# Kernel optimization log

Measured on AMD Instinct MI355X. Metric: run time of the kernel, lower is better.

The kernel has to match this reference:

```python
import jax, jax.numpy as jnp
import numpy as np

B, N, C_SA, OUT = 16, 2048, 512, 1024
BN_EPS = 1e-5


def pconv(x, w, b=None):
    # 1x1 Conv1d: x [B,Cin,N], w [Cout,Cin] -> [B,Cout,N]
    y = jnp.einsum('oc,bcn->bon', w, x)
    return y if b is None else y + b[None, :, None]


def setup_inputs() -> dict:
    key = jax.random.key(0)
    ks = jax.random.split(key, 16)
    s = lambda k, shape: jax.random.normal(k, shape, dtype=jnp.float32) * 0.05
    return {
        'x': jax.random.normal(ks[0], (B, 3, N), dtype=jnp.float32),
        'w1': s(ks[1], (128, 21)), 'b1': s(ks[2], (128,)),
        'w2': s(ks[3], (256, 128)), 'b2': s(ks[4], (256,)),
        'w3': s(ks[5], (512, 512)), 'b3': s(ks[6], (512,)),
        'w4': s(ks[7], (OUT, 512)), 'b4': s(ks[8], (OUT,)),
        'wqk': s(ks[9], (C_SA // 4, C_SA)),            # q_conv.weight tied to k_conv.weight, no bias
        'wv': s(ks[10], (C_SA, C_SA)), 'bv': s(ks[11], (C_SA,)),
        'wt': s(ks[12], (C_SA, C_SA)), 'bt': s(ks[13], (C_SA,)),
        'gamma': jnp.ones((C_SA,), dtype=jnp.float32),
        'beta': jnp.zeros((C_SA,), dtype=jnp.float32),
    }


def reference(x, w1, b1, w2, b2, w3, b3, w4, b4, wqk, wv, bv, wt, bt, gamma, beta):
    b, _, n = x.shape
    # positional encoding on [B,N,3]: [t, sin(t*2^i), cos(t*2^i)] for i in 0..2 -> 21 channels
    t = jnp.transpose(x, (0, 2, 1))
    enc = [t]
    for f in (1.0, 2.0, 4.0):
        enc.append(jnp.sin(t * f))
        enc.append(jnp.cos(t * f))
    h = jnp.transpose(jnp.concatenate(enc, axis=-1), (0, 2, 1))  # [B,21,N]

    h = jax.nn.relu(pconv(h, w1, b1))               # [B,128,N]
    h = pconv(h, w2, b2)                            # [B,256,N]
    g = jnp.max(h, axis=2)                          # [B,256]
    h = jnp.concatenate([h, jnp.broadcast_to(g[:, :, None], (b, g.shape[1], n))], axis=1)  # [B,512,N]
    h = jax.nn.relu(pconv(h, w3, b3))               # [B,512,N]

    # SA_Layer (offset attention, double normalization)
    xq = jnp.einsum('oc,bcn->bno', wqk, h)          # [B,N,128]
    xk = jnp.einsum('oc,bcn->bon', wqk, h)          # [B,128,N]
    xv = pconv(h, wv, bv)                           # [B,512,N]
    energy = jnp.einsum('bqo,bok->bqk', xq, xk)     # [B,N,N]
    attn = jax.nn.softmax(energy, axis=-1)
    attn = attn / (1e-9 + jnp.sum(attn, axis=1, keepdims=True))  # L1 renorm over query dim
    x_r = jnp.einsum('bck,bqk->bcq', xv, attn)      # x_v @ attn^T -> [B,512,N]
    d = pconv(h - x_r, wt, bt)
    # BatchNorm1d, training mode (batch statistics, biased variance)
    mu = jnp.mean(d, axis=(0, 2))
    var = jnp.var(d, axis=(0, 2))
    d = gamma[None, :, None] * (d - mu[None, :, None]) * jax.lax.rsqrt(var + BN_EPS)[None, :, None] + beta[None, :, None]
    h = h + jax.nn.relu(d)

    h = pconv(h, w4, b4)                            # [B,OUT,N]
    return jnp.max(h, axis=2)                       # [B,OUT]
```

## Files before the change

### kernel.cpp

```cpp
#include <hip/hip_runtime.h>
#include <cmath>

#define GN 2048
#define GB 16

typedef __attribute__((ext_vector_type(8))) short bf8_t;
typedef __attribute__((ext_vector_type(4))) float f4_t;

__device__ __forceinline__ short f2bf(float f) {
    union { float f; unsigned u; } v; v.f = f;
    unsigned r = v.u + 0x7FFFu + ((v.u >> 16) & 1u);
    return (short)(r >> 16);
}
__device__ __forceinline__ float bf2f(short s) {
    union { unsigned u; float f; } v; v.u = ((unsigned)(unsigned short)s) << 16;
    return v.f;
}

__device__ __forceinline__ void load16_lds(const short* g, short* l) {
    __builtin_amdgcn_global_load_lds(
        (const __attribute__((address_space(1))) unsigned int*)g,
        (__attribute__((address_space(3))) unsigned int*)l, 16, 0, 0);
}

__device__ __forceinline__ float wave_max(float v) {
#pragma unroll
    for (int o = 32; o > 0; o >>= 1) v = fmaxf(v, __shfl_xor(v, o, 64));
    return v;
}
__device__ __forceinline__ float wave_sum(float v) {
#pragma unroll
    for (int o = 32; o > 0; o >>= 1) v += __shfl_xor(v, o, 64);
    return v;
}
__device__ __forceinline__ float block_sum(float v) {
    __shared__ float sm[4];
    v = wave_sum(v);
    if ((threadIdx.x & 63) == 0) sm[threadIdx.x >> 6] = v;
    __syncthreads();
    v = sm[0] + sm[1] + sm[2] + sm[3];
    __syncthreads();
    return v;
}

__global__ __launch_bounds__(256) void f2ball_k(
    const float* __restrict__ w2, const float* __restrict__ w3,
    const float* __restrict__ wqk, const float* __restrict__ wv,
    const float* __restrict__ wt, const float* __restrict__ w4,
    short* __restrict__ dst) {
    int i = blockIdx.x * 256 + threadIdx.x;
    if (i >= 1409024) return;
    float v;
    if (i < 32768) v = w2[i];
    else if (i < 294912) v = w3[i - 32768];
    else if (i < 360448) v = wqk[i - 294912];
    else if (i < 622592) v = wv[i - 360448];
    else if (i < 884736) v = wt[i - 622592];
    else v = w4[i - 884736];
    dst[i] = f2bf(v);
}

__global__ __launch_bounds__(256) void posenc_conv1_k(
    const float* __restrict__ x, const float* __restrict__ w1,
    const float* __restrict__ b1, short* __restrict__ h1) {
    __shared__ float w[128 * 21];
    __shared__ float bb[128];
    __shared__ float se[256][21];
    const int tid = threadIdx.x;
    for (int i = tid; i < 128 * 21; i += 256) w[i] = w1[i];
    if (tid < 128) bb[tid] = b1[tid];
    int p0 = blockIdx.x * 256;
    int p = p0 + tid, b = p >> 11, n = p & (GN - 1);
    const float* xb = x + (long)b * 3 * GN + n;
    float t0 = xb[0], t1 = xb[GN], t2 = xb[2 * GN];
    se[tid][0] = t0; se[tid][1] = t1; se[tid][2] = t2;
    se[tid][3] = sinf(t0); se[tid][4] = sinf(t1); se[tid][5] = sinf(t2);
    se[tid][6] = cosf(t0); se[tid][7] = cosf(t1); se[tid][8] = cosf(t2);
    se[tid][9] = sinf(2.f * t0); se[tid][10] = sinf(2.f * t1); se[tid][11] = sinf(2.f * t2);
    se[tid][12] = cosf(2.f * t0); se[tid][13] = cosf(2.f * t1); se[tid][14] = cosf(2.f * t2);
    se[tid][15] = sinf(4.f * t0); se[tid][16] = sinf(4.f * t1); se[tid][17] = sinf(4.f * t2);
    se[tid][18] = cosf(4.f * t0); se[tid][19] = cosf(4.f * t1); se[tid][20] = cosf(4.f * t2);
    __syncthreads();
    short* outb = h1 + (long)p0 * 128;
    for (int it = 0; it < 128; ++it) {
        int L = it * 256 + tid;
        int pl = L >> 7, o = L & 127;
        float s = bb[o];
        const float* er = se[pl];
        const float* wr = &w[o * 21];
#pragma unroll
        for (int c = 0; c < 21; ++c) s = fmaf(wr[c], er[c], s);
        outb[L] = f2bf(fmaxf(s, 0.f));
    }
}

template <int MODE, int BIAS, bool RELU, bool STATS = false, bool COLMAX = false>
__global__ __launch_bounds__(256) void mm_k(
    const short* __restrict__ A, int lda, long long aB,
    const short* __restrict__ B, int ldb, long long bB,
    const float* __restrict__ bias, int biasStride,
    const short* __restrict__ aux, long long auxB,
    const float* __restrict__ rsv,
    float* __restrict__ Cf, long long cfB,
    short* __restrict__ Cb, long long cbB,
    float* __restrict__ Pmax, float* __restrict__ Ps2,
    int ldc, int K) {
    const int z = blockIdx.z;
    A += (long long)z * aB;
    B += (long long)z * bB;
    if (MODE == 4) { aux += (long long)z * auxB; rsv += (long long)z * GN; }
    if (MODE == 1) Cf += (long long)z * cfB;
    if (MODE == 2 || MODE == 4 || MODE == 6) Cb += (long long)z * cbB;
    if (MODE == 6) Pmax += (long long)z * GN * 32;
    const int row0 = blockIdx.x * 128, col0 = blockIdx.y * 128;
    const int tid = threadIdx.x;
    const int lane = tid & 63, w = tid >> 6;
    const int r = lane & 15, q = lane >> 4;
    const int wr = w >> 1, wc = w & 1;

    __shared__ short lA[8192];
    __shared__ short lB[8192];

    f4_t acc[4][4] = {};

    const int sRow = lane >> 2;
    const int sKb = (lane & 3) ^ ((lane >> 3) & 3);
    const long aG = (long)(row0 + w * 32 + sRow) * lda + sKb * 8;
    const long bG = (long)(col0 + w * 32 + sRow) * ldb + sKb * 8;
    short* ldsA0 = lA + (w * 32) * 32;
    short* ldsA1 = lA + (w * 32 + 16) * 32;
    short* ldsB0 = lB + (w * 32) * 32;
    short* ldsB1 = lB + (w * 32 + 16) * 32;

    const int sw = (q ^ ((r >> 1) & 3)) * 8;
    int aoff[4], boff[4];
#pragma unroll
    for (int i = 0; i < 4; ++i) {
        aoff[i] = (wr * 64 + i * 16 + r) * 32 + sw;
        boff[i] = (wc * 64 + i * 16 + r) * 32 + sw;
    }

    for (int k0 = 0; k0 < K; k0 += 64) {
        __syncthreads();
        load16_lds(A + aG + k0, ldsA0);
        load16_lds(A + aG + (long)16 * lda + k0, ldsA1);
        load16_lds(B + bG + k0, ldsB0);
        load16_lds(B + bG + (long)16 * ldb + k0, ldsB1);
        load16_lds(A + aG + k0 + 32, ldsA0 + 4096);
        load16_lds(A + aG + (long)16 * lda + k0 + 32, ldsA1 + 4096);
        load16_lds(B + bG + k0 + 32, ldsB0 + 4096);
        load16_lds(B + bG + (long)16 * ldb + k0 + 32, ldsB1 + 4096);
        asm volatile("s_waitcnt vmcnt(0)" ::: "memory");
        __syncthreads();
#pragma unroll
        for (int h = 0; h < 2; ++h) {
            const short* la = lA + h * 4096;
            const short* lb = lB + h * 4096;
            bf8_t av[4], bv[4];
#pragma unroll
            for (int i = 0; i < 4; ++i) av[i] = *(const bf8_t*)(la + aoff[i]);
#pragma unroll
            for (int j = 0; j < 4; ++j) bv[j] = *(const bf8_t*)(lb + boff[j]);
#pragma unroll
            for (int i = 0; i < 4; ++i)
#pragma unroll
                for (int j = 0; j < 4; ++j)
                    acc[i][j] = __builtin_amdgcn_mfma_f32_16x16x32_bf16(av[i], bv[j], acc[i][j], 0, 0, 0);
        }
    }

    if constexpr (MODE == 5) {
        int b = row0 >> 11;
        int rw = (blockIdx.x * 2 + wr) & 31;
#pragma unroll
        for (int j = 0; j < 4; ++j) {
            float vm = -1e30f;
#pragma unroll
            for (int i = 0; i < 4; ++i)
#pragma unroll
                for (int e = 0; e < 4; ++e) vm = fmaxf(vm, acc[i][j][e]);
            vm = fmaxf(vm, __shfl_xor(vm, 16, 64));
            vm = fmaxf(vm, __shfl_xor(vm, 32, 64));
            if (q == 0) {
                int gcol = col0 + wc * 64 + j * 16 + r;
                Pmax[(((long)b * 1024 + gcol) << 5) + rw] = vm + bias[gcol];
            }
        }
    } else if constexpr (MODE == 6) {
        float rsum[4][4] = {};
#pragma unroll
        for (int j = 0; j < 4; ++j) {
            int gcol = col0 + wc * 64 + j * 16 + r;
#pragma unroll
            for (int i = 0; i < 4; ++i) {
#pragma unroll
                for (int e = 0; e < 4; ++e) {
                    int grow = row0 + wr * 64 + i * 16 + q * 4 + e;
                    float ex = __expf(acc[i][j][e]);
                    rsum[i][e] += ex;
                    Cb[(long)grow * ldc + gcol] = f2bf(ex);
                }
            }
        }
#pragma unroll
        for (int i = 0; i < 4; ++i)
#pragma unroll
            for (int e = 0; e < 4; ++e) {
                float v = rsum[i][e];
                v += __shfl_xor(v, 1, 64);
                v += __shfl_xor(v, 2, 64);
                v += __shfl_xor(v, 4, 64);
                v += __shfl_xor(v, 8, 64);
                if (r == 0) {
                    int grow = row0 + wr * 64 + i * 16 + q * 4 + e;
                    Pmax[((long)grow << 5) + blockIdx.y * 2 + wc] = v;
                }
            }
    } else if constexpr (MODE == 4) {
#pragma unroll
        for (int i = 0; i < 4; ++i) {
#pragma unroll
            for (int e = 0; e < 4; ++e) {
                int grow = row0 + wr * 64 + i * 16 + q * 4 + e;
                float rsr = rsv[grow];
                long ob = (long)grow * ldc + col0 + wc * 64 + r;
#pragma unroll
                for (int j = 0; j < 4; ++j) {
                    long off = ob + j * 16;
                    Cb[off] = f2bf(bf2f(aux[off]) - acc[i][j][e] * rsr);
                }
            }
        }
    } else {
        const int b2d = (BIAS == 3) ? (row0 >> 11) : 0;
#pragma unroll
        for (int j = 0; j < 4; ++j) {
            int gcol = col0 + wc * 64 + j * 16 + r;
            float bvv = 0.f;
            if constexpr (BIAS == 1) bvv = bias[gcol];
            if constexpr (BIAS == 3) bvv = bias[b2d * biasStride + gcol];
            float s1 = 0.f, s2 = 0.f;
            float cmx = -1e30f;
#pragma unroll
            for (int i = 0; i < 4; ++i) {
#pragma unroll
                for (int e = 0; e < 4; ++e) {
                    int grow = row0 + wr * 64 + i * 16 + q * 4 + e;
                    float v = acc[i][j][e] + bvv;
                    if constexpr (BIAS == 2) v += bias[grow];
                    if constexpr (RELU) v = fmaxf(v, 0.f);
                    if constexpr (STATS) { s1 += v; s2 = fmaf(v, v, s2); }
                    if constexpr (COLMAX) cmx = fmaxf(cmx, v);
                    long off = (long)grow * ldc + gcol;
                    if constexpr (MODE == 1) Cf[off] = v;
                    if constexpr (MODE == 2) Cb[off] = f2bf(v);
                }
            }
            if constexpr (STATS) {
                s1 += __shfl_xor(s1, 16, 64); s1 += __shfl_xor(s1, 32, 64);
                s2 += __shfl_xor(s2, 16, 64); s2 += __shfl_xor(s2, 32, 64);
                if (q == 0) {
                    int rw2 = blockIdx.x * 2 + wr;
                    Pmax[rw2 * 512 + gcol] = s1;
                    Ps2[rw2 * 512 + gcol] = s2;
                }
            }
            if constexpr (COLMAX) {
                cmx = fmaxf(cmx, __shfl_xor(cmx, 16, 64));
                cmx = fmaxf(cmx, __shfl_xor(cmx, 32, 64));
                if (q == 0) {
                    int b = row0 >> 11;
                    int rw = (blockIdx.x * 2 + wr) & 31;
                    Pmax[(((long)b * ldc + gcol) << 5) + rw] = cmx;
                }
            }
        }
    }
}

__device__ __forceinline__ void stage2(const short* g0, const short* g1, short* dst) {
    load16_lds(g0, dst);
    load16_lds(g1, dst + 4096);
}

template <int MH, int NH>
__device__ __forceinline__ void mfma_quad(const bf8_t (&av)[4][2], const bf8_t (&bv)[2][2],
                                          f4_t (&acc)[8][4]) {
#pragma unroll
    for (int mi = 0; mi < 4; ++mi)
#pragma unroll
        for (int ni = 0; ni < 2; ++ni) {
            acc[MH * 4 + mi][NH * 2 + ni] = __builtin_amdgcn_mfma_f32_16x16x32_bf16(
                av[mi][0], bv[ni][0], acc[MH * 4 + mi][NH * 2 + ni], 0, 0, 0);
            acc[MH * 4 + mi][NH * 2 + ni] = __builtin_amdgcn_mfma_f32_16x16x32_bf16(
                av[mi][1], bv[ni][1], acc[MH * 4 + mi][NH * 2 + ni], 0, 0, 0);
        }
}

__device__ __forceinline__ void rd4(const short* p, int swz0, int swz1, bf8_t (&v)[4][2]) {
#pragma unroll
    for (int i = 0; i < 4; ++i) {
        v[i][0] = *(const bf8_t*)(p + i * 1024 + swz0);
        v[i][1] = *(const bf8_t*)(p + i * 1024 + swz1);
    }
}
__device__ __forceinline__ void rd2(const short* p, int swz0, int swz1, bf8_t (&v)[2][2]) {
#pragma unroll
    for (int i = 0; i < 2; ++i) {
        v[i][0] = *(const bf8_t*)(p + i * 1024 + swz0);
        v[i][1] = *(const bf8_t*)(p + i * 1024 + swz1);
    }
}

#define SB0 __builtin_amdgcn_sched_barrier(0)
#define BARRIER asm volatile("s_barrier" ::: "memory")

template <int MODE, int BIAS, bool RELU, bool STATS = false, bool SWZ = false>
__global__ __launch_bounds__(512, 2) void mm256_k(
    const short* __restrict__ A, int lda, long long aB,
    const short* __restrict__ B, int ldb, long long bB,
    const float* __restrict__ bias, int biasStride,
    const short* __restrict__ aux, long long auxB,
    const float* __restrict__ rsv,
    short* __restrict__ Cb, long long cbB,
    float* __restrict__ Pmax, float* __restrict__ Ps2,
    int ldc, int K) {
    __shared__ short lA[32768];
    __shared__ short lB[32768];
    int bx = blockIdx.x, by = blockIdx.y, bz = blockIdx.z;
    if constexpr (SWZ) {
        const int nwg = gridDim.x * gridDim.y * gridDim.z;
        const int bid = bx + gridDim.x * (by + gridDim.y * bz);
        const int cpx = nwg >> 3;
        const int wg = (bid & 7) * cpx + (bid >> 3);
        bx = wg % gridDim.x;
        const int t2 = wg / gridDim.x;
        by = t2 % gridDim.y;
        bz = t2 / gridDim.y;
    }
    const int z = bz;
    A += (long long)z * aB;
    B += (long long)z * bB;
    if constexpr (MODE == 4) { aux += (long long)z * auxB; rsv += (long long)z * GN; }
    if constexpr (MODE != 5) Cb += (long long)z * cbB;
    const int row0 = bx * 256, col0 = by * 256;
    const int tid = threadIdx.x;
    const int lane = tid & 63, w = tid >> 6;
    const int r16 = lane & 15, q = lane >> 4;
    const int wr = w >> 2, wc = w & 3;

    const int rc0 = w * 8 + (lane >> 3);
    const int s8 = ((lane & 7) ^ (rc0 & 7)) * 8;
    const long ldA64 = (long)64 * lda, ldB64 = (long)64 * ldb;
    const short* aH0 = A + (long)(row0 + rc0) * lda + s8;
    const short* aH1 = aH0 + (long)128 * lda;
    const short* bH0 = B + (long)(col0 + rc0) * ldb + s8;
    const short* bH1 = bH0 + (long)128 * ldb;
    short* dA = lA + w * 512;
    short* dB = lB + w * 512;

#define STG_A(d_, h_, kt_) stage2((h_ ? aH1 : aH0) + (long)(kt_) * 64,                      \
                                  (h_ ? aH1 : aH0) + (long)(kt_) * 64 + ldA64,              \
                                  dA + (d_) * 16384 + (h_) * 8192)
#define STG_B(d_, h_, kt_) stage2((h_ ? bH1 : bH0) + (long)(kt_) * 64,                      \
                                  (h_ ? bH1 : bH0) + (long)(kt_) * 64 + ldB64,              \
                                  dB + (d_) * 16384 + (h_) * 8192)

    const int swz0 = (q ^ (r16 & 7)) * 8;
    const int swz1 = ((4 + q) ^ (r16 & 7)) * 8;
    const int arow = (wr * 64 + r16) * 64;
    const int brow = (wc * 32 + r16) * 64;

    f4_t acc[8][4] = {};
    bf8_t av[4][2], bv0[2][2], bv1[2][2];
    const int NT = K >> 6;

    STG_A(0, 0, 0); STG_B(0, 0, 0); STG_B(0, 1, 0); STG_A(0, 1, 0);
    STG_A(1, 0, 1); STG_B(1, 0, 1);
    asm volatile("s_waitcnt vmcnt(4)" ::: "memory");
    SB0; BARRIER; SB0;

    for (int t = 0; t < NT; ++t) {
        const int d = t & 1;
        const short* la = lA + d * 16384;
        const short* lb = lB + d * 16384;
        rd4(la + arow, swz0, swz1, av);
        rd2(lb + brow, swz0, swz1, bv0);
        if (t + 1 < NT) STG_B(d ^ 1, 1, t + 1);
        SB0; BARRIER; SB0;
        __builtin_amdgcn_s_setprio(1);
        mfma_quad<0, 0>(av, bv0, acc);
        __builtin_amdgcn_s_setprio(0);
        SB0; BARRIER; SB0;
        rd2(lb + 8192 + brow, swz0, swz1, bv1);
        if (t + 1 < NT) STG_A(d ^ 1, 1, t + 1);
        SB0; BARRIER; SB0;
        __builtin_amdgcn_s_setprio(1);
        mfma_quad<0, 1>(av, bv1, acc);
        __builtin_amdgcn_s_setprio(0);
        SB0; BARRIER; SB0;
        rd4(la + 8192 + arow, swz0, swz1, av);
        if (t + 2 < NT) STG_A(d, 0, t + 2);
        SB0; BARRIER; SB0;
        __builtin_amdgcn_s_setprio(1);
        mfma_quad<1, 0>(av, bv0, acc);
        __builtin_amdgcn_s_setprio(0);
        SB0; BARRIER; SB0;
        if (t + 2 < NT) {
            STG_B(d, 0, t + 2);
            asm volatile("s_waitcnt vmcnt(4)" ::: "memory");
        } else if (t + 1 < NT) {
            asm volatile("s_waitcnt vmcnt(0)" ::: "memory");
        }
        SB0; BARRIER; SB0;
        __builtin_amdgcn_s_setprio(1);
        mfma_quad<1, 1>(av, bv1, acc);
        __builtin_amdgcn_s_setprio(0);
        SB0; BARRIER; SB0;
    }
#undef STG_A
#undef STG_B

    const int mrow = row0 + wr * 64 + q * 4;
    const int ncol = col0 + wc * 32 + r16;

    if constexpr (MODE == 4) {
#pragma unroll
        for (int m = 0; m < 8; ++m) {
#pragma unroll
            for (int e = 0; e < 4; ++e) {
                const int grow = mrow + (m >> 2) * 128 + (m & 3) * 16 + e;
                const float rsr = rsv[grow];
                const long rb = (long)grow * ldc;
#pragma unroll
                for (int n = 0; n < 4; ++n) {
                    const long off = rb + ncol + (n >> 1) * 128 + (n & 1) * 16;
                    Cb[off] = f2bf(bf2f(aux[off]) - acc[m][n][e] * rsr);
                }
            }
        }
    } else if constexpr (MODE == 2) {
        const int b2d = (BIAS == 3) ? (row0 >> 11) : 0;
#pragma unroll
        for (int n = 0; n < 4; ++n) {
            const int gcol = ncol + (n >> 1) * 128 + (n & 1) * 16;
            float bvv = 0.f;
            if constexpr (BIAS == 1) bvv = bias[gcol];
            if constexpr (BIAS == 3) bvv = bias[b2d * biasStride + gcol];
#pragma unroll
            for (int mh = 0; mh < 2; ++mh) {
                float s1 = 0.f, s2 = 0.f;
#pragma unroll
                for (int mi = 0; mi < 4; ++mi) {
#pragma unroll
                    for (int e = 0; e < 4; ++e) {
                        const int grow = mrow + mh * 128 + mi * 16 + e;
                        float v = acc[mh * 4 + mi][n][e] + bvv;
                        if constexpr (BIAS == 2) v += bias[grow];
                        if constexpr (RELU) v = fmaxf(v, 0.f);
                        if constexpr (STATS) { s1 += v; s2 = fmaf(v, v, s2); }
                        Cb[(long)grow * ldc + gcol] = f2bf(v);
                    }
                }
                if constexpr (STATS) {
                    s1 += __shfl_xor(s1, 16, 64); s1 += __shfl_xor(s1, 32, 64);
                    s2 += __shfl_xor(s2, 16, 64); s2 += __shfl_xor(s2, 32, 64);
                    if (q == 0) {
                        const int rw2 = bx * 4 + mh * 2 + wr;
                        Pmax[rw2 * 512 + gcol] = s1;
                        Ps2[rw2 * 512 + gcol] = s2;
                    }
                }
            }
        }
    } else if constexpr (MODE == 5) {
        const int b = row0 >> 11;
#pragma unroll
        for (int n = 0; n < 4; ++n) {
            const int gcol = ncol + (n >> 1) * 128 + (n & 1) * 16;
            const float bvv = bias[gcol];
#pragma unroll
            for (int mh = 0; mh < 2; ++mh) {
                float vm = -1e30f;
#pragma unroll
                for (int mi = 0; mi < 4; ++mi)
#pragma unroll
                    for (int e = 0; e < 4; ++e) vm = fmaxf(vm, acc[mh * 4 + mi][n][e]);
                vm = fmaxf(vm, __shfl_xor(vm, 16, 64));
                vm = fmaxf(vm, __shfl_xor(vm, 32, 64));
                if (q == 0) {
                    const int rw = (bx * 4 + mh * 2 + wr) & 31;
                    Pmax[(((long)b * ldc + gcol) << 5) + rw] = vm + bvv;
                }
            }
        }
    }
}
#undef SB0
#undef BARRIER

__global__ __launch_bounds__(256) void rs_k(const float* __restrict__ rp,
                                            float* __restrict__ rs) {
    int i = blockIdx.x * 256 + threadIdx.x;
    const float* p = rp + ((long)i << 5);
    float s = 0.f;
#pragma unroll
    for (int j = 0; j < 32; ++j) s += p[j];
    rs[i] = 1.f / s;
}

__global__ __launch_bounds__(256) void maxg_k(const float* __restrict__ P,
                                              float* __restrict__ g) {
    int i = blockIdx.x * 256 + threadIdx.x;
    const float* p = P + ((long)i << 5);
    float m = p[0];
#pragma unroll
    for (int j = 1; j < 32; ++j) m = fmaxf(m, p[j]);
    g[i] = m;
}

__global__ __launch_bounds__(256) void cvec_k(const float* __restrict__ w3,
                                              const float* __restrict__ b3,
                                              const float* __restrict__ g,
                                              float* __restrict__ cvec) {
    int idx = blockIdx.x * 256 + threadIdx.x;
    int b = idx >> 9, o = idx & 511;
    const float* gb = g + (b << 8);
    const float* wr = w3 + (long)o * 512 + 256;
    float s = b3[o];
    for (int c = 0; c < 256; ++c) s = fmaf(wr[c], gb[c], s);
    cvec[idx] = s;
}

__global__ __launch_bounds__(256) void colsum1_k(const short* __restrict__ Ab,
                                                 const float* __restrict__ rs,
                                                 float* __restrict__ cp) {
    const int qs = blockIdx.x, z = blockIdx.y;
    const int k0 = threadIdx.x * 8;
    const short* p = Ab + (long)z * GN * GN + (long)qs * 64 * GN + k0;
    const float* rv = rs + z * GN + qs * 64;
    float s[8] = {};
    for (int qq = 0; qq < 64; ++qq) {
        uint4 v = *(const uint4*)(p + (long)qq * GN);
        const float rr = rv[qq];
        const short* sp = (const short*)&v;
#pragma unroll
        for (int j = 0; j < 8; ++j) s[j] = fmaf(bf2f(sp[j]), rr, s[j]);
    }
    float* o = cp + ((long)(z * 32 + qs) * GN) + k0;
#pragma unroll
    for (int j = 0; j < 8; ++j) o[j] = s[j];
}
__global__ __launch_bounds__(256) void colsum2_k(const float* __restrict__ cp,
                                                 float* __restrict__ cs) {
    int k = blockIdx.x * 256 + threadIdx.x, z = blockIdx.y;
    float s = 1e-9f;
    for (int qs = 0; qs < 32; ++qs) s += cp[((z * 32 + qs) * GN) + k];
    cs[z * GN + k] = s;
}

__global__ __launch_bounds__(256) void xvscale_k(short* __restrict__ xvc,
                                                 const float* __restrict__ cs) {
    long idx = ((long)blockIdx.x * 256 + threadIdx.x) * 4;
    int p = (int)(idx & 32767);
    short* ptr = xvc + idx;
    float4 cv = *(const float4*)(cs + p);
    uint2 u = *(const uint2*)ptr;
    short* sp = (short*)&u;
    sp[0] = f2bf(bf2f(sp[0]) / cv.x);
    sp[1] = f2bf(bf2f(sp[1]) / cv.y);
    sp[2] = f2bf(bf2f(sp[2]) / cv.z);
    sp[3] = f2bf(bf2f(sp[3]) / cv.w);
    *(uint2*)ptr = u;
}

__global__ __launch_bounds__(256) void bn2_k(const float* __restrict__ bs1,
                                             const float* __restrict__ bs2,
                                             const float* __restrict__ gamma,
                                             const float* __restrict__ beta,
                                             float* __restrict__ sc,
                                             float* __restrict__ sh) {
    int c = blockIdx.x;
    float s = 0.f, s2 = 0.f;
    for (int i = threadIdx.x; i < 512; i += 256) {
        s += bs1[i * 512 + c];
        s2 += bs2[i * 512 + c];
    }
    s = block_sum(s);
    s2 = block_sum(s2);
    if (threadIdx.x == 0) {
        const float cnt = (float)(GB * GN);
        float mu = s / cnt;
        float var = s2 / cnt - mu * mu;
        float r = rsqrtf(var + 1e-5f);
        float gm = gamma[c] * r;
        sc[c] = gm;
        sh[c] = beta[c] - gm * mu;
    }
}

__global__ __launch_bounds__(256) void bn_apply_k(const short* __restrict__ h3b,
                                                  const short* __restrict__ d,
                                                  const float* __restrict__ sc,
                                                  const float* __restrict__ sh,
                                                  short* __restrict__ h4) {
    long bidx = ((long)blockIdx.x * 256 + threadIdx.x) * 4;
    int c = (int)(bidx & 511);
    uint2 du = *(const uint2*)(d + bidx);
    short* ds = (short*)&du;
    uint2 hu = *(const uint2*)(h3b + bidx);
    short* hs = (short*)&hu;
    float4 a4 = *(const float4*)(sc + c);
    float4 b4 = *(const float4*)(sh + c);
    float r0 = bf2f(hs[0]) + fmaxf(fmaf(bf2f(ds[0]), a4.x, b4.x), 0.f);
    float r1 = bf2f(hs[1]) + fmaxf(fmaf(bf2f(ds[1]), a4.y, b4.y), 0.f);
    float r2 = bf2f(hs[2]) + fmaxf(fmaf(bf2f(ds[2]), a4.z, b4.z), 0.f);
    float r3 = bf2f(hs[3]) + fmaxf(fmaf(bf2f(ds[3]), a4.w, b4.w), 0.f);
    uint2 o;
    o.x = (unsigned short)f2bf(r0) | ((unsigned)(unsigned short)f2bf(r1) << 16);
    o.y = (unsigned short)f2bf(r2) | ((unsigned)(unsigned short)f2bf(r3) << 16);
    *(uint2*)(h4 + bidx) = o;
}

__global__ __launch_bounds__(256) void max_final_k(const float* __restrict__ P,
                                                   float* __restrict__ out) {
    int i = blockIdx.x * 256 + threadIdx.x;
    const float* p = P + ((long)i << 5);
    float m = p[0];
#pragma unroll
    for (int j = 1; j < 32; ++j) m = fmaxf(m, p[j]);
    out[i] = m;
}

extern "C" void kernel_launch(void* const* d_in, const int* in_sizes, int n_in,
                              void* d_out, int out_size, void* d_ws, size_t ws_size,
                              hipStream_t stream) {
    const float* x = (const float*)d_in[0];
    const float* w1 = (const float*)d_in[1];
    const float* b1 = (const float*)d_in[2];
    const float* w2 = (const float*)d_in[3];
    const float* b2 = (const float*)d_in[4];
    const float* w3 = (const float*)d_in[5];
    const float* b3 = (const float*)d_in[6];
    const float* w4 = (const float*)d_in[7];
    const float* b4 = (const float*)d_in[8];
    const float* wqk = (const float*)d_in[9];
    const float* wv = (const float*)d_in[10];
    const float* bv = (const float*)d_in[11];
    const float* wt = (const float*)d_in[12];
    const float* bt = (const float*)d_in[13];
    const float* gamma = (const float*)d_in[14];
    const float* beta = (const float*)d_in[15];
    float* out = (float*)d_out;

    char* base = (char*)d_ws;
    short* h3b = (short*)base;
    short* hsT = (short*)(base + 33554432);
    short* kT  = (short*)(base + 67108864);
    short* xvc = (short*)(base + 75497472);
    short* EA  = (short*)(base + 109051904);
    short* h1T = (short*)(base + 109051904);
    short* h2T = (short*)(base + 117440512);
    short* dTb = (short*)(base + 109051904);
    short* h4T = (short*)(base + 67108864);
    char* S = base + 243269632;
    float* g    = (float*)(S + 262144);
    float* cvec = (float*)(S + 278528);
    float* cp   = (float*)(S + 311296);
    float* rp   = cp;
    float* cs   = (float*)(S + 4505600);
    float* bs1  = (float*)(S + 4636672);
    float* bs2  = (float*)(S + 5685248);
    float* bnsc = (float*)(S + 6733824);
    float* bnsh = (float*)(S + 6735872);
    float* Pmax = (float*)(S + 6737920);
    short* w2b  = (short*)(S + 8835072);
    short* w3b  = (short*)(S + 8900608);
    short* wqkb = (short*)(S + 9424896);
    short* wvb  = (short*)(S + 9555968);
    short* wtb  = (short*)(S + 10080256);
    short* w4b  = (short*)(S + 10604544);
    float* rs   = (float*)(S + 11653120);

    f2ball_k<<<5505, 256, 0, stream>>>(w2, w3, wqk, wv, wt, w4, w2b);

    posenc_conv1_k<<<128, 256, 0, stream>>>(x, w1, b1, h1T);

    mm_k<2, 1, false, false, true><<<dim3(256, 2, 1), 256, 0, stream>>>(
        h1T, 128, 0, w2b, 128, 0, b2, 0, nullptr, 0, nullptr,
        nullptr, 0, h2T, 0, Pmax, nullptr, 256, 128);

    maxg_k<<<16, 256, 0, stream>>>(Pmax, g);

    cvec_k<<<32, 256, 0, stream>>>(w3, b3, g, cvec);

    mm256_k<2, 3, true><<<dim3(128, 2, 1), 512, 0, stream>>>(
        h2T, 256, 0, w3b, 512, 0, cvec, 512, nullptr, 0, nullptr,
        h3b, 0, nullptr, nullptr, 512, 256);

    mm_k<2, 0, false><<<dim3(256, 1, 1), 256, 0, stream>>>(
        h3b, 512, 0, wqkb, 512, 0, nullptr, 0, nullptr, 0, nullptr,
        nullptr, 0, kT, 0, nullptr, nullptr, 128, 512);

    mm256_k<2, 2, false><<<dim3(2, 128, 1), 512, 0, stream>>>(
        wvb, 512, 0, h3b, 512, 0, bv, 0, nullptr, 0, nullptr,
        xvc, 0, nullptr, nullptr, 32768, 512);

    mm_k<6, 0, false><<<dim3(16, 16, 16), 256, 0, stream>>>(
        kT, 128, (long long)GN * 128, kT, 128, (long long)GN * 128,
        nullptr, 0, nullptr, 0, nullptr, nullptr, 0,
        EA, (long long)GN * GN, rp, nullptr, GN, 128);
    rs_k<<<128, 256, 0, stream>>>(rp, rs);
    colsum1_k<<<dim3(32, GB), 256, 0, stream>>>(EA, rs, cp);
    colsum2_k<<<dim3(8, GB), 256, 0, stream>>>(cp, cs);
    xvscale_k<<<16384, 256, 0, stream>>>(xvc, cs);
    mm256_k<4, 0, false, false, true><<<dim3(8, 2, 16), 512, 0, stream>>>(
        EA, GN, (long long)GN * GN,
        xvc, 32768, (long long)GN,
        nullptr, 0, h3b, (long long)GN * 512, rs,
        hsT, (long long)GN * 512, nullptr, nullptr, 512, GN);

    mm256_k<2, 1, false, true><<<dim3(128, 2, 1), 512, 0, stream>>>(
        hsT, 512, 0, wtb, 512, 0, bt, 0, nullptr, 0, nullptr,
        dTb, 0, bs1, bs2, 512, 512);

    bn2_k<<<512, 256, 0, stream>>>(bs1, bs2, gamma, beta, bnsc, bnsh);

    bn_apply_k<<<16384, 256, 0, stream>>>(h3b, dTb, bnsc, bnsh, h4T);

    mm256_k<5, 1, false><<<dim3(128, 4, 1), 512, 0, stream>>>(
        h4T, 512, 0, w4b, 512, 0, b4, 0, nullptr, 0, nullptr,
        nullptr, 0, Pmax, nullptr, 1024, 512);

    max_final_k<<<64, 256, 0, stream>>>(Pmax, out);
}
```

Before: 476.5 us.

## Collapse mm256 pipeline to two phases, drop block swizzle, use mm_k for two GEMMs

Restructures the 256x256 GEMM main loop so all B fragments are read up front and the four MFMA quadrants run in two barrier-separated phases instead of four, halving the number of s_barriers per K-tile. Staging of the next tiles is batched into the same phases, and a guard handles the single-tile case. The XCD-aware block-index swizzle is removed. The h3 and xv GEMMs move back to the smaller-tile mm_k kernel for more blocks. Fewer barriers reduce sync overhead, but the changes lower load/MFMA interleaving, raise register pressure, and lose L2 locality from the swizzle.

```diff
diff --git a/kernel.cpp b/kernel.cpp
--- a/kernel.cpp
+++ b/kernel.cpp
@@ -315,7 +315,7 @@
 #define SB0 __builtin_amdgcn_sched_barrier(0)
 #define BARRIER asm volatile("s_barrier" ::: "memory")
 
-template <int MODE, int BIAS, bool RELU, bool STATS = false, bool SWZ = false>
+template <int MODE, int BIAS, bool RELU, bool STATS = false>
 __global__ __launch_bounds__(512, 2) void mm256_k(
     const short* __restrict__ A, int lda, long long aB,
     const short* __restrict__ B, int ldb, long long bB,
@@ -327,17 +327,7 @@
     int ldc, int K) {
     __shared__ short lA[32768];
     __shared__ short lB[32768];
-    int bx = blockIdx.x, by = blockIdx.y, bz = blockIdx.z;
-    if constexpr (SWZ) {
-        const int nwg = gridDim.x * gridDim.y * gridDim.z;
-        const int bid = bx + gridDim.x * (by + gridDim.y * bz);
-        const int cpx = nwg >> 3;
-        const int wg = (bid & 7) * cpx + (bid >> 3);
-        bx = wg % gridDim.x;
-        const int t2 = wg / gridDim.x;
-        by = t2 % gridDim.y;
-        bz = t2 / gridDim.y;
-    }
+    const int bx = blockIdx.x, by = blockIdx.y, bz = blockIdx.z;
     const int z = bz;
     A += (long long)z * aB;
     B += (long long)z * bB;
@@ -375,9 +365,13 @@
     bf8_t av[4][2], bv0[2][2], bv1[2][2];
     const int NT = K >> 6;
 
-    STG_A(0, 0, 0); STG_B(0, 0, 0); STG_B(0, 1, 0); STG_A(0, 1, 0);
-    STG_A(1, 0, 1); STG_B(1, 0, 1);
-    asm volatile("s_waitcnt vmcnt(4)" ::: "memory");
+    STG_A(0, 0, 0); STG_B(0, 0, 0); STG_A(0, 1, 0); STG_B(0, 1, 0);
+    if (NT > 1) {
+        STG_A(1, 0, 1); STG_B(1, 0, 1);
+        asm volatile("s_waitcnt vmcnt(4)" ::: "memory");
+    } else {
+        asm volatile("s_waitcnt vmcnt(0)" ::: "memory");
+    }
     SB0; BARRIER; SB0;
 
     for (int t = 0; t < NT; ++t) {
@@ -386,34 +380,24 @@
         const short* lb = lB + d * 16384;
         rd4(la + arow, swz0, swz1, av);
         rd2(lb + brow, swz0, swz1, bv0);
-        if (t + 1 < NT) STG_B(d ^ 1, 1, t + 1);
+        rd2(lb + 8192 + brow, swz0, swz1, bv1);
+        if (t + 1 < NT) { STG_A(d ^ 1, 1, t + 1); STG_B(d ^ 1, 1, t + 1); }
         SB0; BARRIER; SB0;
         __builtin_amdgcn_s_setprio(1);
         mfma_quad<0, 0>(av, bv0, acc);
-        __builtin_amdgcn_s_setprio(0);
-        SB0; BARRIER; SB0;
-        rd2(lb + 8192 + brow, swz0, swz1, bv1);
-        if (t + 1 < NT) STG_A(d ^ 1, 1, t + 1);
-        SB0; BARRIER; SB0;
-        __builtin_amdgcn_s_setprio(1);
         mfma_quad<0, 1>(av, bv1, acc);
         __builtin_amdgcn_s_setprio(0);
         SB0; BARRIER; SB0;
         rd4(la + 8192 + arow, swz0, swz1, av);
-        if (t + 2 < NT) STG_A(d, 0, t + 2);
+        if (t + 2 < NT) {
+            STG_A(d, 0, t + 2); STG_B(d, 0, t + 2);
+            asm volatile("s_waitcnt vmcnt(4)" ::: "memory");
+        } else if (t + 1 < NT) {
+            asm volatile("s_waitcnt vmcnt(0)" ::: "memory");
+        }
         SB0; BARRIER; SB0;
         __builtin_amdgcn_s_setprio(1);
         mfma_quad<1, 0>(av, bv0, acc);
-        __builtin_amdgcn_s_setprio(0);
-        SB0; BARRIER; SB0;
-        if (t + 2 < NT) {
-            STG_B(d, 0, t + 2);
-            asm volatile("s_waitcnt vmcnt(4)" ::: "memory");
-        } else if (t + 1 < NT) {
-            asm volatile("s_waitcnt vmcnt(0)" ::: "memory");
-        }
-        SB0; BARRIER; SB0;
-        __builtin_amdgcn_s_setprio(1);
         mfma_quad<1, 1>(av, bv1, acc);
         __builtin_amdgcn_s_setprio(0);
         SB0; BARRIER; SB0;
@@ -694,17 +678,17 @@
 
     cvec_k<<<32, 256, 0, stream>>>(w3, b3, g, cvec);
 
-    mm256_k<2, 3, true><<<dim3(128, 2, 1), 512, 0, stream>>>(
+    mm_k<2, 3, true><<<dim3(256, 4, 1), 256, 0, stream>>>(
         h2T, 256, 0, w3b, 512, 0, cvec, 512, nullptr, 0, nullptr,
-        h3b, 0, nullptr, nullptr, 512, 256);
+        nullptr, 0, h3b, 0, nullptr, nullptr, 512, 256);
 
     mm_k<2, 0, false><<<dim3(256, 1, 1), 256, 0, stream>>>(
         h3b, 512, 0, wqkb, 512, 0, nullptr, 0, nullptr, 0, nullptr,
         nullptr, 0, kT, 0, nullptr, nullptr, 128, 512);
 
-    mm256_k<2, 2, false><<<dim3(2, 128, 1), 512, 0, stream>>>(
+    mm_k<2, 2, false><<<dim3(4, 256, 1), 256, 0, stream>>>(
         wvb, 512, 0, h3b, 512, 0, bv, 0, nullptr, 0, nullptr,
-        xvc, 0, nullptr, nullptr, 32768, 512);
+        nullptr, 0, xvc, 0, nullptr, nullptr, 32768, 512);
 
     mm_k<6, 0, false><<<dim3(16, 16, 16), 256, 0, stream>>>(
         kT, 128, (long long)GN * 128, kT, 128, (long long)GN * 128,
@@ -714,7 +698,7 @@
     colsum1_k<<<dim3(32, GB), 256, 0, stream>>>(EA, rs, cp);
     colsum2_k<<<dim3(8, GB), 256, 0, stream>>>(cp, cs);
     xvscale_k<<<16384, 256, 0, stream>>>(xvc, cs);
-    mm256_k<4, 0, false, false, true><<<dim3(8, 2, 16), 512, 0, stream>>>(
+    mm256_k<4, 0, false><<<dim3(8, 2, 16), 512, 0, stream>>>(
         EA, GN, (long long)GN * GN,
         xvc, 32768, (long long)GN,
         nullptr, 0, h3b, (long long)GN * 512, rs,
```

Result: faster. 461.5 us (-3.2%).
